# Kernel tuning notes

Measured on AMD Instinct MI355X. Metric: run time of the kernel, lower is better.

## Reference

```python
import jax, jax.numpy as jnp
import numpy as np

EPS = 1e-5
SCALE = 30.0

def _ln(x, g, b):
    m = jnp.mean(x, axis=-1, keepdims=True)
    v = jnp.mean((x - m) ** 2, axis=-1, keepdims=True)
    return (x - m) * jax.lax.rsqrt(v + EPS) * g + b

def setup_inputs() -> dict:
    key = jax.random.key(0)
    ks = jax.random.split(key, 12)
    B, L, K, H, NIN = 4, 2048, 48, 128, 512
    s = 0.02
    return {
        "h_V": jax.random.normal(ks[0], (B, L, H), jnp.float32),
        "h_E": jax.random.normal(ks[1], (B, L, K, NIN - H), jnp.float32),
        "mask_V": jnp.ones((B, L), jnp.float32),
        "mask_E": jnp.ones((B, L, K), jnp.float32),
        "w1": jax.random.normal(ks[2], (NIN, H), jnp.float32) * s,
        "b1": jnp.zeros((H,), jnp.float32),
        "w2": jax.random.normal(ks[3], (H, H), jnp.float32) * s,
        "b2": jnp.zeros((H,), jnp.float32),
        "w3": jax.random.normal(ks[4], (H, H), jnp.float32) * s,
        "b3": jnp.zeros((H,), jnp.float32),
        "g1": jnp.ones((H,), jnp.float32),
        "bn1": jnp.zeros((H,), jnp.float32),
        "g2": jnp.ones((H,), jnp.float32),
        "bn2": jnp.zeros((H,), jnp.float32),
        "wf1": jax.random.normal(ks[5], (H, 4 * H), jnp.float32) * s,
        "bf1": jnp.zeros((4 * H,), jnp.float32),
        "wf2": jax.random.normal(ks[6], (4 * H, H), jnp.float32) * s,
        "bf2": jnp.zeros((H,), jnp.float32),
    }

def reference(h_V, h_E, mask_V, mask_E, w1, b1, w2, b2, w3, b3, g1, bn1, g2, bn2, wf1, bf1, wf2, bf2):
    B, L, H = h_V.shape
    K = h_E.shape[-2]
    gelu = lambda x: jax.nn.gelu(x, approximate=False)  # torch nn.GELU default (erf)
    # expand source node over K neighbors and concat: (B,L,K,num_in)
    h_V_exp = jnp.broadcast_to(h_V[:, :, None, :], (B, L, K, H))
    h_EV = jnp.concatenate([h_V_exp, h_E], axis=-1)
    h_msg = gelu(jnp.einsum('blki,ih->blkh', h_EV, w1) + b1)
    h_msg = gelu(jnp.einsum('blkh,hj->blkj', h_msg, w2) + b2)
    h_msg = jnp.einsum('blkh,hj->blkj', h_msg, w3) + b3
    h_msg = mask_E[..., None] * h_msg
    dh = jnp.sum(h_msg, axis=-2) / SCALE  # masked sum-aggregate over K
    h = _ln(h_V + dh, g1, bn1)
    dff = jnp.einsum('blh,hf->blf', h, wf1) + bf1
    dff = jnp.einsum('blf,fh->blh', gelu(dff), wf2) + bf2
    h = _ln(h + dff, g2, bn2)
    return mask_V[..., None] * h
```

## Files before the change

kernel.cpp:

```cpp
#include <hip/hip_runtime.h>
#include <hip/hip_bf16.h>


typedef __bf16 bf16x8 __attribute__((ext_vector_type(8)));
typedef __bf16 bf16x4 __attribute__((ext_vector_type(4)));
typedef float f32x4 __attribute__((ext_vector_type(4)));

#define HH 128
#define EE 384
#define KK 48

__device__ __forceinline__ float gelu_f(float x) {
  float x2 = x * x;
  float u = x * (-1.5957691216f - 0.0713548163f * x2);
  float e = __expf(u);
  return __fdividef(x, 1.0f + e);
}

__device__ __forceinline__ bf16x8 cvt8v(f32x4 a, f32x4 b) {
  bf16x8 r;
  #pragma unroll
  for (int i = 0; i < 4; ++i) { r[i] = (__bf16)a[i]; r[i + 4] = (__bf16)b[i]; }
  return r;
}

__device__ __forceinline__ f32x4 mfma16(bf16x8 a, bf16x8 b, f32x4 c) {
  return __builtin_amdgcn_mfma_f32_16x16x32_bf16(a, b, c, 0, 0, 0);
}

__device__ __forceinline__ void gload16(const void* g, void* l) {
  __builtin_amdgcn_global_load_lds(
      (const __attribute__((address_space(1))) void*)g,
      (__attribute__((address_space(3))) void*)l, 16, 0, 0);
}

__global__ void prep_kernel(const float* __restrict__ w1, const float* __restrict__ w2,
                            const float* __restrict__ w3, const float* __restrict__ wf1,
                            const float* __restrict__ wf2, __bf16* __restrict__ out) {
  int idx = blockIdx.x * 256 + threadIdx.x;
  if (idx < 49152) {
    int t = idx & 7, lane = (idx >> 3) & 63, n = (idx >> 9) & 7, kc = idx >> 12;
    int e = kc * 32 + (lane >> 4) * 8 + t, h = n * 16 + (lane & 15);
    out[idx] = (__bf16)w1[(128 + e) * 128 + h];
  } else if (idx < 65536) {
    int u = idx - 49152;
    int t = u & 7, lane = (u >> 3) & 63, n = (u >> 9) & 7, kc = u >> 12;
    int e = kc * 32 + (lane >> 4) * 8 + t, h = n * 16 + (lane & 15);
    out[idx] = (__bf16)w2[e * 128 + h];
  } else if (idx < 81920) {
    int u = idx - 65536;
    int t = u & 7, lane = (u >> 3) & 63, n = (u >> 9) & 7, kc = u >> 12;
    int e = kc * 32 + (lane >> 4) * 8 + t, h = n * 16 + (lane & 15);
    out[idx] = (__bf16)w3[e * 128 + h];
  } else if (idx < 147456) {
    int u = idx - 81920;
    int t = u & 7, lane = (u >> 3) & 63, n = (u >> 9) & 7, kc = (u >> 12) & 3, w = u >> 14;
    int f = w * 128 + n * 16 + (lane & 15), h = kc * 32 + (lane >> 4) * 8 + t;
    out[idx] = (__bf16)wf1[h * 512 + f];
  } else if (idx < 212992) {
    int u = idx - 147456;
    int t = u & 7, lane = (u >> 3) & 63, n = (u >> 9) & 1, kc = (u >> 10) & 15, w = u >> 14;
    int j = w * 32 + n * 16 + (lane & 15), f = kc * 32 + (lane >> 4) * 8 + t;
    out[idx] = (__bf16)wf2[f * 128 + j];
  }
}

__global__ __launch_bounds__(128) void v1_kernel(const float* __restrict__ hV,
                                                 const float* __restrict__ w1,
                                                 const float* __restrict__ b1,
                                                 float* __restrict__ V1) {
  __shared__ __align__(16) float sV[16][128];
  const int tid = threadIdx.x;
  const long p0 = (long)blockIdx.x * 16;
  for (int i = 0; i < 16; ++i) sV[i][tid] = hV[(p0 + i) * HH + tid];
  __syncthreads();
  float acc[16];
  float bb = b1[tid];
  #pragma unroll
  for (int p = 0; p < 16; ++p) acc[p] = bb;
  for (int k = 0; k < 128; k += 4) {
    float wa = w1[(k + 0) * HH + tid];
    float wb = w1[(k + 1) * HH + tid];
    float wc = w1[(k + 2) * HH + tid];
    float wd = w1[(k + 3) * HH + tid];
    #pragma unroll
    for (int p = 0; p < 16; ++p) {
      float4 h4 = *(const float4*)&sV[p][k];
      acc[p] = fmaf(h4.x, wa, fmaf(h4.y, wb, fmaf(h4.z, wc, fmaf(h4.w, wd, acc[p]))));
    }
  }
  #pragma unroll
  for (int p = 0; p < 16; ++p) V1[(p0 + p) * HH + tid] = acc[p];
}

__global__ __launch_bounds__(256, 3) void msg_kernel(
    const float* __restrict__ hE, const float* __restrict__ hV,
    const float* __restrict__ maskE,
    const __bf16* __restrict__ w1f, const __bf16* __restrict__ w2f,
    const __bf16* __restrict__ w3f, const float* __restrict__ V1,
    const float* __restrict__ b2, const float* __restrict__ b3,
    const float* __restrict__ g1, const float* __restrict__ bn1,
    float* __restrict__ outH) {
  __shared__ __align__(16) char sBuf[3][12288];
  __shared__ __align__(16) float sBias[512];
  __shared__ __align__(16) float sPart[4][2];

  const int tid = threadIdx.x;
  const int lane = tid & 63;
  const int w = tid >> 6;
  const int fr = lane & 15;
  const int fg = lane >> 4;
  const long p = blockIdx.x;

  for (int j = tid; j < 512; j += 256) {
    float v;
    if (j < 128) v = b2[j];
    else if (j < 256) v = b3[j - 128];
    else if (j < 384) v = g1[j - 256];
    else v = bn1[j - 384];
    sBias[j] = v;
  }
  __syncthreads();

  const float mk0 = maskE[p * KK + fr];
  const float mk1 = maskE[p * KK + 16 + fr];
  const float mk2 = maskE[p * KK + 32 + fr];

  const char* hEp = (const char*)(hE + p * (long)(KK * EE));
  const int lrow = lane >> 4;
  const int lcb = (lane & 15) * 16;
  const int r0 = (w * 3 + 0) * 4 + lrow;
  const int r1 = (w * 3 + 1) * 4 + lrow;
  const int r2 = (w * 3 + 2) * 4 + lrow;
  const char* srcA0 = hEp + r0 * 1536 + (lcb ^ ((r0 & 7) << 5));
  const char* srcA1 = hEp + r1 * 1536 + (lcb ^ ((r1 & 7) << 5));
  const char* srcA2 = hEp + r2 * 1536 + (lcb ^ ((r2 & 7) << 5));
  const int dst0 = (w * 3 + 0) * 1024;
  const int dst1 = (w * 3 + 1) * 1024;
  const int dst2 = (w * 3 + 2) * 1024;

  const __bf16* b1base = w1f + (2 * w) * 512 + lane * 8;
  const __bf16* b2base = w2f + (2 * w) * 512 + lane * 8;
  const __bf16* b3base = w3f + (2 * w) * 512 + lane * 8;

  const int aswz = (fr & 7) << 5;
  const int hswz = (fr & 7) << 4;
  char* hB = &sBuf[0][0];

  f32x4 acc[3][2];
  #pragma unroll
  for (int m = 0; m < 3; ++m)
    #pragma unroll
    for (int n = 0; n < 2; ++n) acc[m][n] = (f32x4){0.f, 0.f, 0.f, 0.f};

  bf16x8 Bs0[2], Bs1[2], Bs2[2], Bs3[2];

#define STAGE(C, BUF) { \
    gload16(srcA0 + (C) * 256, &sBuf[BUF][0] + dst0); \
    gload16(srcA1 + (C) * 256, &sBuf[BUF][0] + dst1); \
    gload16(srcA2 + (C) * 256, &sBuf[BUF][0] + dst2); }
#define LOADB(SET, BASE, KC) { \
    SET[0] = *(const bf16x8*)((BASE) + (KC) * 4096); \
    SET[1] = *(const bf16x8*)((BASE) + (KC) * 4096 + 256); }
#define WAITV(N) asm volatile("s_waitcnt vmcnt(" #N ")" ::: "memory")
#define BAR      asm volatile("s_barrier" ::: "memory")
#define BARL     asm volatile("s_waitcnt lgkmcnt(0)\ns_barrier" ::: "memory")

#define KSTEP(BUF, KS, SET) { \
    const char* rb_ = &sBuf[BUF][0]; \
    const int cb_ = ((KS) * 128 + fg * 32) ^ aswz; \
    f32x4 x0_ = *(const f32x4*)(rb_ + fr * 256 + cb_); \
    f32x4 x1_ = *(const f32x4*)(rb_ + fr * 256 + cb_ + 16); \
    f32x4 x2_ = *(const f32x4*)(rb_ + (16 + fr) * 256 + cb_); \
    f32x4 x3_ = *(const f32x4*)(rb_ + (16 + fr) * 256 + cb_ + 16); \
    f32x4 x4_ = *(const f32x4*)(rb_ + (32 + fr) * 256 + cb_); \
    f32x4 x5_ = *(const f32x4*)(rb_ + (32 + fr) * 256 + cb_ + 16); \
    bf16x8 af0 = cvt8v(x0_, x1_); \
    bf16x8 af1 = cvt8v(x2_, x3_); \
    bf16x8 af2 = cvt8v(x4_, x5_); \
    acc[0][0] = mfma16(SET[0], af0, acc[0][0]); acc[0][1] = mfma16(SET[1], af0, acc[0][1]); \
    acc[1][0] = mfma16(SET[0], af1, acc[1][0]); acc[1][1] = mfma16(SET[1], af1, acc[1][1]); \
    acc[2][0] = mfma16(SET[0], af2, acc[2][0]); acc[2][1] = mfma16(SET[1], af2, acc[2][1]); }

#define KSTEPH(KS, SET) { \
    const int cb_ = ((KS) * 64 + fg * 16) ^ hswz; \
    bf16x8 af0 = *(const bf16x8*)(hB + fr * 256 + cb_); \
    bf16x8 af1 = *(const bf16x8*)(hB + (16 + fr) * 256 + cb_); \
    bf16x8 af2 = *(const bf16x8*)(hB + (32 + fr) * 256 + cb_); \
    acc[0][0] = mfma16(SET[0], af0, acc[0][0]); acc[0][1] = mfma16(SET[1], af0, acc[0][1]); \
    acc[1][0] = mfma16(SET[0], af1, acc[1][0]); acc[1][1] = mfma16(SET[1], af1, acc[1][1]); \
    acc[2][0] = mfma16(SET[0], af2, acc[2][0]); acc[2][1] = mfma16(SET[1], af2, acc[2][1]); }

#define EPI(BQ0, BQ1) { \
    _Pragma("unroll") for (int m_ = 0; m_ < 3; ++m_) { \
      const int rb_ = (m_ * 16 + fr) * 256; \
      { bf16x4 t_; \
        _Pragma("unroll") for (int j_ = 0; j_ < 4; ++j_) t_[j_] = (__bf16)gelu_f(acc[m_][0][j_] + BQ0[j_]); \
        *(bf16x4*)(hB + rb_ + (((2 * w) * 32 + fg * 8) ^ hswz)) = t_; \
        acc[m_][0] = (f32x4){0.f, 0.f, 0.f, 0.f}; } \
      { bf16x4 t_; \
        _Pragma("unroll") for (int j_ = 0; j_ < 4; ++j_) t_[j_] = (__bf16)gelu_f(acc[m_][1][j_] + BQ1[j_]); \
        *(bf16x4*)(hB + rb_ + (((2 * w + 1) * 32 + fg * 8) ^ hswz)) = t_; \
        acc[m_][1] = (f32x4){0.f, 0.f, 0.f, 0.f}; } } }

  STAGE(0, 0);
  LOADB(Bs0, b1base, 0);
  LOADB(Bs1, b1base, 1);
  STAGE(1, 1);
  LOADB(Bs2, b1base, 2);
  LOADB(Bs3, b1base, 3);

  f32x4 vq0, vq1, hq0, hq1;

  WAITV(7); BAR;
  KSTEP(0, 0, Bs0); LOADB(Bs0, b1base, 4);
  KSTEP(0, 1, Bs1); LOADB(Bs1, b1base, 5);
  STAGE(2, 2);

  WAITV(7); BAR;
  KSTEP(1, 0, Bs2); LOADB(Bs2, b1base, 6);
  KSTEP(1, 1, Bs3); LOADB(Bs3, b1base, 7);
  STAGE(3, 0);

  WAITV(7); BAR;
  KSTEP(2, 0, Bs0); LOADB(Bs0, b1base, 8);
  KSTEP(2, 1, Bs1); LOADB(Bs1, b1base, 9);
  STAGE(4, 1);

  WAITV(7); BAR;
  KSTEP(0, 0, Bs2); LOADB(Bs2, b1base, 10);
  KSTEP(0, 1, Bs3); LOADB(Bs3, b1base, 11);
  STAGE(5, 2);

  WAITV(7); BAR;
  KSTEP(1, 0, Bs0); LOADB(Bs0, b2base, 0);
  vq0 = *(const f32x4*)(V1 + p * HH + (2 * w) * 16 + fg * 4);
  vq1 = *(const f32x4*)(V1 + p * HH + (2 * w + 1) * 16 + fg * 4);
  KSTEP(1, 1, Bs1); LOADB(Bs1, b2base, 1);

  WAITV(6); BAR;
  KSTEP(2, 0, Bs2); LOADB(Bs2, b2base, 2);
  KSTEP(2, 1, Bs3); LOADB(Bs3, b2base, 3);

  WAITV(4);
  EPI(vq0, vq1);
  BARL;

  KSTEPH(0, Bs0); LOADB(Bs0, b3base, 0);
  KSTEPH(1, Bs1); LOADB(Bs1, b3base, 1);
  WAITV(4);
  KSTEPH(2, Bs2); LOADB(Bs2, b3base, 2);
  KSTEPH(3, Bs3); LOADB(Bs3, b3base, 3);
  BARL;
  {
    f32x4 bq0 = *(const f32x4*)(&sBias[(2 * w) * 16 + fg * 4]);
    f32x4 bq1 = *(const f32x4*)(&sBias[(2 * w + 1) * 16 + fg * 4]);
    EPI(bq0, bq1);
  }
  BARL;

  WAITV(6);
  KSTEPH(0, Bs0);
  hq0 = *(const f32x4*)(hV + p * HH + (2 * w) * 16 + fg * 4);
  hq1 = *(const f32x4*)(hV + p * HH + (2 * w + 1) * 16 + fg * 4);
  KSTEPH(1, Bs1);
  WAITV(4);
  KSTEPH(2, Bs2);
  KSTEPH(3, Bs3);

  f32x4 red[2];
  {
    #pragma unroll
    for (int n = 0; n < 2; ++n) {
      f32x4 bq = *(const f32x4*)(&sBias[128 + (2 * w + n) * 16 + fg * 4]);
      red[n] = mk0 * (acc[0][n] + bq) + mk1 * (acc[1][n] + bq) + mk2 * (acc[2][n] + bq);
    }
    #pragma unroll
    for (int off = 1; off <= 8; off <<= 1)
      #pragma unroll
      for (int n = 0; n < 2; ++n)
        #pragma unroll
        for (int j = 0; j < 4; ++j)
          red[n][j] += __shfl_xor(red[n][j], off);
  }

  WAITV(0);
  {
    f32x4 xq[2];
    xq[0] = hq0 + red[0] * (1.f / 30.f);
    xq[1] = hq1 + red[1] * (1.f / 30.f);
    float s = 0.f, t = 0.f;
    #pragma unroll
    for (int n = 0; n < 2; ++n)
      #pragma unroll
      for (int j = 0; j < 4; ++j) { float x = xq[n][j]; s += x; t += x * x; }
    s += __shfl_xor(s, 16); s += __shfl_xor(s, 32);
    t += __shfl_xor(t, 16); t += __shfl_xor(t, 32);
    if (lane == 0) { sPart[w][0] = s; sPart[w][1] = t; }
    BARL;
    float S = sPart[0][0] + sPart[1][0] + sPart[2][0] + sPart[3][0];
    float T = sPart[0][1] + sPart[1][1] + sPart[2][1] + sPart[3][1];
    float mean = S * (1.f / 128.f);
    float var = T * (1.f / 128.f) - mean * mean;
    float rs = rsqrtf(var + 1e-5f);
    if (fr == 0) {
      #pragma unroll
      for (int n = 0; n < 2; ++n) {
        f32x4 gq = *(const f32x4*)(&sBias[256 + (2 * w + n) * 16 + fg * 4]);
        f32x4 bq = *(const f32x4*)(&sBias[384 + (2 * w + n) * 16 + fg * 4]);
        f32x4 o;
        #pragma unroll
        for (int j = 0; j < 4; ++j) o[j] = (xq[n][j] - mean) * rs * gq[j] + bq[j];
        *(f32x4*)(outH + p * HH + (2 * w + n) * 16 + fg * 4) = o;
      }
    }
  }
#undef STAGE
#undef LOADB
#undef WAITV
#undef BAR
#undef BARL
#undef KSTEP
#undef KSTEPH
#undef EPI
}

__global__ __launch_bounds__(256, 2) void ffn_kernel(
    const float* __restrict__ xin, const __bf16* __restrict__ wf1g,
    const float* __restrict__ bf1, const __bf16* __restrict__ wf2g,
    const float* __restrict__ bf2, const float* __restrict__ g2,
    const float* __restrict__ bn2, const float* __restrict__ maskV,
    float* __restrict__ out) {
  __shared__ __align__(16) __bf16 sX[16][136];
  __shared__ __align__(16) __bf16 sH1[16][520];
  __shared__ __align__(16) float sOut[16][132];
  const int tid = threadIdx.x, lane = tid & 63, w = tid >> 6;
  const long row0 = (long)blockIdx.x * 16;
  const int fr = lane & 15, fg = lane >> 4;
  const __bf16* bw1 = wf1g + w * 16384 + lane * 8;
  const __bf16* bw2 = wf2g + w * 16384 + lane * 8;

  {
    int r = tid >> 4, c = (tid & 15) * 8;
    const float* src = xin + (row0 + r) * HH + c;
    f32x4 v0 = *(const f32x4*)src, v1 = *(const f32x4*)(src + 4);
    *(bf16x8*)&sX[r][c] = cvt8v(v0, v1);
  }
  __syncthreads();

  f32x4 a1[8];
  #pragma unroll
  for (int n = 0; n < 8; ++n) a1[n] = (f32x4){0.f, 0.f, 0.f, 0.f};
  #pragma unroll
  for (int kc = 0; kc < 4; ++kc) {
    int k0 = kc * 32;
    bf16x8 af0 = *(const bf16x8*)&sX[fr][k0 + fg * 8];
    #pragma unroll
    for (int n = 0; n < 8; ++n) {
      bf16x8 bfr = *(const bf16x8*)(bw1 + (kc * 8 + n) * 512);
      a1[n] = mfma16(af0, bfr, a1[n]);
    }
  }
  #pragma unroll
  for (int n = 0; n < 8; ++n) {
    float bv = bf1[w * 128 + n * 16 + fr];
    #pragma unroll
    for (int j = 0; j < 4; ++j)
      sH1[fg * 4 + j][w * 128 + n * 16 + fr] = (__bf16)gelu_f(a1[n][j] + bv);
  }
  __syncthreads();

  f32x4 a2[2];
  #pragma unroll
  for (int n = 0; n < 2; ++n) a2[n] = (f32x4){0.f, 0.f, 0.f, 0.f};
  #pragma unroll
  for (int kc = 0; kc < 16; ++kc) {
    int k0 = kc * 32;
    bf16x8 af0 = *(const bf16x8*)&sH1[fr][k0 + fg * 8];
    #pragma unroll
    for (int n = 0; n < 2; ++n) {
      bf16x8 bfr = *(const bf16x8*)(bw2 + (kc * 2 + n) * 512);
      a2[n] = mfma16(af0, bfr, a2[n]);
    }
  }
  #pragma unroll
  for (int n = 0; n < 2; ++n) {
    float bv = bf2[w * 32 + n * 16 + fr];
    #pragma unroll
    for (int j = 0; j < 4; ++j)
      sOut[fg * 4 + j][w * 32 + n * 16 + fr] = a2[n][j] + bv;
  }
  __syncthreads();

  {
    int r = tid >> 4, c0 = (tid & 15) * 8;
    long p = row0 + r;
    const float* xp = xin + p * HH + c0;
    float x[8];
    #pragma unroll
    for (int i = 0; i < 8; ++i) x[i] = xp[i] + sOut[r][c0 + i];
    float s = 0.f;
    #pragma unroll
    for (int i = 0; i < 8; ++i) s += x[i];
    s += __shfl_xor(s, 1); s += __shfl_xor(s, 2); s += __shfl_xor(s, 4); s += __shfl_xor(s, 8);
    float mean = s * (1.f / 128.f);
    float q = 0.f;
    #pragma unroll
    for (int i = 0; i < 8; ++i) { float e = x[i] - mean; q += e * e; }
    q += __shfl_xor(q, 1); q += __shfl_xor(q, 2); q += __shfl_xor(q, 4); q += __shfl_xor(q, 8);
    float rs = rsqrtf(q * (1.f / 128.f) + 1e-5f);
    float mv = maskV[p];
    float* op = out + p * HH + c0;
    #pragma unroll
    for (int i = 0; i < 8; ++i)
      op[i] = ((x[i] - mean) * rs * g2[c0 + i] + bn2[c0 + i]) * mv;
  }
}

extern "C" void kernel_launch(void* const* d_in, const int* in_sizes, int n_in,
                              void* d_out, int out_size, void* d_ws, size_t ws_size,
                              hipStream_t stream) {
  const float* hV    = (const float*)d_in[0];
  const float* hE    = (const float*)d_in[1];
  const float* maskV = (const float*)d_in[2];
  const float* maskE = (const float*)d_in[3];
  const float* w1    = (const float*)d_in[4];
  const float* b1    = (const float*)d_in[5];
  const float* w2    = (const float*)d_in[6];
  const float* b2    = (const float*)d_in[7];
  const float* w3    = (const float*)d_in[8];
  const float* b3    = (const float*)d_in[9];
  const float* g1    = (const float*)d_in[10];
  const float* bn1   = (const float*)d_in[11];
  const float* g2    = (const float*)d_in[12];
  const float* bn2   = (const float*)d_in[13];
  const float* wf1   = (const float*)d_in[14];
  const float* bf1   = (const float*)d_in[15];
  const float* wf2   = (const float*)d_in[16];
  const float* bf2   = (const float*)d_in[17];
  float* out = (float*)d_out;

  __bf16* wsb = (__bf16*)d_ws;
  float* V1   = (float*)((char*)d_ws + 425984);
  float* hbuf = (float*)((char*)d_ws + 4620288);

  prep_kernel<<<832, 256, 0, stream>>>(w1, w2, w3, wf1, wf2, wsb);
  v1_kernel<<<512, 128, 0, stream>>>(hV, w1, b1, V1);
  msg_kernel<<<8192, 256, 0, stream>>>(hE, hV, maskE,
                                       wsb, wsb + 49152, wsb + 65536, V1,
                                       b2, b3, g1, bn1, hbuf);
  ffn_kernel<<<512, 256, 0, stream>>>(hbuf, wsb + 81920, bf1, wsb + 147456, bf2,
                                      g2, bn2, maskV, out);
}
```

Before: 201.5 us.

## Process two nodes per msg block, prefetching second node's edges during first's tail

Each msg_kernel block now handles two consecutive nodes instead of one, halving the grid. The second node's h_E tiles are staged into the free LDS buffers while the first node's W2/W3 layers and LayerNorm run, so the global-load pipeline is not drained between nodes. LayerNorm switches from a one-pass E[x^2]-mean^2 variance to a two-pass centered variance, which adds an extra barrier. The hand-tuned vmcnt waits become more intricate, and the smaller grid means fewer blocks to spread across CUs.

```diff
diff --git a/kernel.cpp b/kernel.cpp
--- a/kernel.cpp
+++ b/kernel.cpp
@@ -110,7 +110,8 @@
   const int w = tid >> 6;
   const int fr = lane & 15;
   const int fg = lane >> 4;
-  const long p = blockIdx.x;
+  const long p0 = (long)blockIdx.x * 2;
+  const long p1 = p0 + 1;
 
   for (int j = tid; j < 512; j += 256) {
     float v;
@@ -122,11 +123,7 @@
   }
   __syncthreads();
 
-  const float mk0 = maskE[p * KK + fr];
-  const float mk1 = maskE[p * KK + 16 + fr];
-  const float mk2 = maskE[p * KK + 32 + fr];
-
-  const char* hEp = (const char*)(hE + p * (long)(KK * EE));
+  const char* hEp = (const char*)(hE + p0 * (long)(KK * EE));
   const int lrow = lane >> 4;
   const int lcb = (lane & 15) * 16;
   const int r0 = (w * 3 + 0) * 4 + lrow;
@@ -138,6 +135,7 @@
   const int dst0 = (w * 3 + 0) * 1024;
   const int dst1 = (w * 3 + 1) * 1024;
   const int dst2 = (w * 3 + 2) * 1024;
+  const int DP = KK * EE * 4;
 
   const __bf16* b1base = w1f + (2 * w) * 512 + lane * 8;
   const __bf16* b2base = w2f + (2 * w) * 512 + lane * 8;
@@ -145,7 +143,6 @@
 
   const int aswz = (fr & 7) << 5;
   const int hswz = (fr & 7) << 4;
-  char* hB = &sBuf[0][0];
 
   f32x4 acc[3][2];
   #pragma unroll
@@ -154,11 +151,12 @@
     for (int n = 0; n < 2; ++n) acc[m][n] = (f32x4){0.f, 0.f, 0.f, 0.f};
 
   bf16x8 Bs0[2], Bs1[2], Bs2[2], Bs3[2];
-
-#define STAGE(C, BUF) { \
-    gload16(srcA0 + (C) * 256, &sBuf[BUF][0] + dst0); \
-    gload16(srcA1 + (C) * 256, &sBuf[BUF][0] + dst1); \
-    gload16(srcA2 + (C) * 256, &sBuf[BUF][0] + dst2); }
+  float mk0, mk1, mk2;
+
+#define STAGE(POFF, C, BUF) { \
+    gload16(srcA0 + (POFF) + (C) * 256, &sBuf[BUF][0] + dst0); \
+    gload16(srcA1 + (POFF) + (C) * 256, &sBuf[BUF][0] + dst1); \
+    gload16(srcA2 + (POFF) + (C) * 256, &sBuf[BUF][0] + dst2); }
 #define LOADB(SET, BASE, KC) { \
     SET[0] = *(const bf16x8*)((BASE) + (KC) * 4096); \
     SET[1] = *(const bf16x8*)((BASE) + (KC) * 4096 + 256); }
@@ -182,139 +180,180 @@
     acc[1][0] = mfma16(SET[0], af1, acc[1][0]); acc[1][1] = mfma16(SET[1], af1, acc[1][1]); \
     acc[2][0] = mfma16(SET[0], af2, acc[2][0]); acc[2][1] = mfma16(SET[1], af2, acc[2][1]); }
 
-#define KSTEPH(KS, SET) { \
+#define KSTEPH(HB, KS, SET) { \
     const int cb_ = ((KS) * 64 + fg * 16) ^ hswz; \
-    bf16x8 af0 = *(const bf16x8*)(hB + fr * 256 + cb_); \
-    bf16x8 af1 = *(const bf16x8*)(hB + (16 + fr) * 256 + cb_); \
-    bf16x8 af2 = *(const bf16x8*)(hB + (32 + fr) * 256 + cb_); \
+    bf16x8 af0 = *(const bf16x8*)((HB) + fr * 256 + cb_); \
+    bf16x8 af1 = *(const bf16x8*)((HB) + (16 + fr) * 256 + cb_); \
+    bf16x8 af2 = *(const bf16x8*)((HB) + (32 + fr) * 256 + cb_); \
     acc[0][0] = mfma16(SET[0], af0, acc[0][0]); acc[0][1] = mfma16(SET[1], af0, acc[0][1]); \
     acc[1][0] = mfma16(SET[0], af1, acc[1][0]); acc[1][1] = mfma16(SET[1], af1, acc[1][1]); \
     acc[2][0] = mfma16(SET[0], af2, acc[2][0]); acc[2][1] = mfma16(SET[1], af2, acc[2][1]); }
 
-#define EPI(BQ0, BQ1) { \
+#define EPI(HB, BQ0, BQ1) { \
     _Pragma("unroll") for (int m_ = 0; m_ < 3; ++m_) { \
       const int rb_ = (m_ * 16 + fr) * 256; \
       { bf16x4 t_; \
         _Pragma("unroll") for (int j_ = 0; j_ < 4; ++j_) t_[j_] = (__bf16)gelu_f(acc[m_][0][j_] + BQ0[j_]); \
-        *(bf16x4*)(hB + rb_ + (((2 * w) * 32 + fg * 8) ^ hswz)) = t_; \
+        *(bf16x4*)((HB) + rb_ + (((2 * w) * 32 + fg * 8) ^ hswz)) = t_; \
         acc[m_][0] = (f32x4){0.f, 0.f, 0.f, 0.f}; } \
       { bf16x4 t_; \
         _Pragma("unroll") for (int j_ = 0; j_ < 4; ++j_) t_[j_] = (__bf16)gelu_f(acc[m_][1][j_] + BQ1[j_]); \
-        *(bf16x4*)(hB + rb_ + (((2 * w + 1) * 32 + fg * 8) ^ hswz)) = t_; \
+        *(bf16x4*)((HB) + rb_ + (((2 * w + 1) * 32 + fg * 8) ^ hswz)) = t_; \
         acc[m_][1] = (f32x4){0.f, 0.f, 0.f, 0.f}; } } }
 
-  STAGE(0, 0);
+#define REDLN(PP) { \
+    f32x4 red[2]; \
+    _Pragma("unroll") for (int n_ = 0; n_ < 2; ++n_) { \
+      f32x4 bq_ = *(const f32x4*)(&sBias[128 + (2 * w + n_) * 16 + fg * 4]); \
+      red[n_] = mk0 * (acc[0][n_] + bq_) + mk1 * (acc[1][n_] + bq_) + mk2 * (acc[2][n_] + bq_); \
+      acc[0][n_] = (f32x4){0.f, 0.f, 0.f, 0.f}; \
+      acc[1][n_] = (f32x4){0.f, 0.f, 0.f, 0.f}; \
+      acc[2][n_] = (f32x4){0.f, 0.f, 0.f, 0.f}; } \
+    _Pragma("unroll") for (int off_ = 1; off_ <= 8; off_ <<= 1) \
+      _Pragma("unroll") for (int n_ = 0; n_ < 2; ++n_) \
+        _Pragma("unroll") for (int j_ = 0; j_ < 4; ++j_) \
+          red[n_][j_] += __shfl_xor(red[n_][j_], off_); \
+    f32x4 xq[2]; \
+    xq[0] = hq0 + red[0] * (1.f / 30.f); \
+    xq[1] = hq1 + red[1] * (1.f / 30.f); \
+    float s_ = 0.f; \
+    _Pragma("unroll") for (int n_ = 0; n_ < 2; ++n_) \
+      _Pragma("unroll") for (int j_ = 0; j_ < 4; ++j_) s_ += xq[n_][j_]; \
+    s_ += __shfl_xor(s_, 16); s_ += __shfl_xor(s_, 32); \
+    if (lane == 0) sPart[w][0] = s_; \
+    BARL; \
+    float mean_ = (sPart[0][0] + sPart[1][0] + sPart[2][0] + sPart[3][0]) * (1.f / 128.f); \
+    float q_ = 0.f; \
+    _Pragma("unroll") for (int n_ = 0; n_ < 2; ++n_) \
+      _Pragma("unroll") for (int j_ = 0; j_ < 4; ++j_) { float e_ = xq[n_][j_] - mean_; q_ += e_ * e_; } \
+    q_ += __shfl_xor(q_, 16); q_ += __shfl_xor(q_, 32); \
+    if (lane == 0) sPart[w][1] = q_; \
+    BARL; \
+    float var_ = (sPart[0][1] + sPart[1][1] + sPart[2][1] + sPart[3][1]) * (1.f / 128.f); \
+    float rs_ = rsqrtf(var_ + 1e-5f); \
+    if (fr == 0) { \
+      _Pragma("unroll") for (int n_ = 0; n_ < 2; ++n_) { \
+        f32x4 gq_ = *(const f32x4*)(&sBias[256 + (2 * w + n_) * 16 + fg * 4]); \
+        f32x4 bq_ = *(const f32x4*)(&sBias[384 + (2 * w + n_) * 16 + fg * 4]); \
+        f32x4 o_; \
+        _Pragma("unroll") for (int j_ = 0; j_ < 4; ++j_) \
+          o_[j_] = (xq[n_][j_] - mean_) * rs_ * gq_[j_] + bq_[j_]; \
+        *(f32x4*)(outH + (PP) * HH + (2 * w + n_) * 16 + fg * 4) = o_; } } }
+
+  f32x4 vq0, vq1, hq0, hq1;
+
+  mk0 = maskE[p0 * KK + fr]; mk1 = maskE[p0 * KK + 16 + fr]; mk2 = maskE[p0 * KK + 32 + fr];
+  STAGE(0, 0, 0);
   LOADB(Bs0, b1base, 0);
   LOADB(Bs1, b1base, 1);
-  STAGE(1, 1);
+  STAGE(0, 1, 1);
   LOADB(Bs2, b1base, 2);
   LOADB(Bs3, b1base, 3);
 
-  f32x4 vq0, vq1, hq0, hq1;
-
   WAITV(7); BAR;
   KSTEP(0, 0, Bs0); LOADB(Bs0, b1base, 4);
   KSTEP(0, 1, Bs1); LOADB(Bs1, b1base, 5);
-  STAGE(2, 2);
-
+  STAGE(0, 2, 2);
   WAITV(7); BAR;
   KSTEP(1, 0, Bs2); LOADB(Bs2, b1base, 6);
   KSTEP(1, 1, Bs3); LOADB(Bs3, b1base, 7);
-  STAGE(3, 0);
-
+  STAGE(0, 3, 0);
   WAITV(7); BAR;
   KSTEP(2, 0, Bs0); LOADB(Bs0, b1base, 8);
   KSTEP(2, 1, Bs1); LOADB(Bs1, b1base, 9);
-  STAGE(4, 1);
-
+  STAGE(0, 4, 1);
   WAITV(7); BAR;
   KSTEP(0, 0, Bs2); LOADB(Bs2, b1base, 10);
   KSTEP(0, 1, Bs3); LOADB(Bs3, b1base, 11);
-  STAGE(5, 2);
-
+  STAGE(0, 5, 2);
   WAITV(7); BAR;
   KSTEP(1, 0, Bs0); LOADB(Bs0, b2base, 0);
-  vq0 = *(const f32x4*)(V1 + p * HH + (2 * w) * 16 + fg * 4);
-  vq1 = *(const f32x4*)(V1 + p * HH + (2 * w + 1) * 16 + fg * 4);
+  vq0 = *(const f32x4*)(V1 + p0 * HH + (2 * w) * 16 + fg * 4);
+  vq1 = *(const f32x4*)(V1 + p0 * HH + (2 * w + 1) * 16 + fg * 4);
   KSTEP(1, 1, Bs1); LOADB(Bs1, b2base, 1);
-
   WAITV(6); BAR;
   KSTEP(2, 0, Bs2); LOADB(Bs2, b2base, 2);
   KSTEP(2, 1, Bs3); LOADB(Bs3, b2base, 3);
 
-  WAITV(4);
-  EPI(vq0, vq1);
-  BARL;
-
-  KSTEPH(0, Bs0); LOADB(Bs0, b3base, 0);
-  KSTEPH(1, Bs1); LOADB(Bs1, b3base, 1);
-  WAITV(4);
-  KSTEPH(2, Bs2); LOADB(Bs2, b3base, 2);
-  KSTEPH(3, Bs3); LOADB(Bs3, b3base, 3);
+  WAITV(6);
+  EPI(&sBuf[0][0], vq0, vq1);
+  BARL;
+  STAGE(DP, 0, 1);
+
+  KSTEPH(&sBuf[0][0], 0, Bs0); LOADB(Bs0, b3base, 0);
+  hq0 = *(const f32x4*)(hV + p0 * HH + (2 * w) * 16 + fg * 4);
+  hq1 = *(const f32x4*)(hV + p0 * HH + (2 * w + 1) * 16 + fg * 4);
+  WAITV(11); KSTEPH(&sBuf[0][0], 1, Bs1); LOADB(Bs1, b3base, 1);
+  WAITV(11); KSTEPH(&sBuf[0][0], 2, Bs2); LOADB(Bs2, b3base, 2);
+  WAITV(11); KSTEPH(&sBuf[0][0], 3, Bs3); LOADB(Bs3, b3base, 3);
   BARL;
   {
     f32x4 bq0 = *(const f32x4*)(&sBias[(2 * w) * 16 + fg * 4]);
     f32x4 bq1 = *(const f32x4*)(&sBias[(2 * w + 1) * 16 + fg * 4]);
-    EPI(bq0, bq1);
-  }
-  BARL;
+    EPI(&sBuf[0][0], bq0, bq1);
+  }
+  BARL;
+  STAGE(DP, 1, 2);
+
+  WAITV(11); KSTEPH(&sBuf[0][0], 0, Bs0); LOADB(Bs0, b1base, 0);
+  WAITV(9);  KSTEPH(&sBuf[0][0], 1, Bs1); LOADB(Bs1, b1base, 1);
+  WAITV(9);  KSTEPH(&sBuf[0][0], 2, Bs2); LOADB(Bs2, b1base, 2);
+  WAITV(9);  KSTEPH(&sBuf[0][0], 3, Bs3); LOADB(Bs3, b1base, 3);
+
+  REDLN(p0);
+
+  mk0 = maskE[p1 * KK + fr]; mk1 = maskE[p1 * KK + 16 + fr]; mk2 = maskE[p1 * KK + 32 + fr];
+  STAGE(DP, 2, 0);
+
+  WAITV(10); BAR;
+  KSTEP(1, 0, Bs0); LOADB(Bs0, b1base, 4);
+  KSTEP(1, 1, Bs1); LOADB(Bs1, b1base, 5);
+  WAITV(10); BAR;
+  KSTEP(2, 0, Bs2); LOADB(Bs2, b1base, 6);
+  KSTEP(2, 1, Bs3); LOADB(Bs3, b1base, 7);
+  STAGE(DP, 3, 1);
+  WAITV(7); BAR;
+  KSTEP(0, 0, Bs0); LOADB(Bs0, b1base, 8);
+  KSTEP(0, 1, Bs1); LOADB(Bs1, b1base, 9);
+  STAGE(DP, 4, 2);
+  WAITV(7); BAR;
+  KSTEP(1, 0, Bs2); LOADB(Bs2, b1base, 10);
+  KSTEP(1, 1, Bs3); LOADB(Bs3, b1base, 11);
+  STAGE(DP, 5, 0);
+  WAITV(7); BAR;
+  KSTEP(2, 0, Bs0); LOADB(Bs0, b2base, 0);
+  vq0 = *(const f32x4*)(V1 + p1 * HH + (2 * w) * 16 + fg * 4);
+  vq1 = *(const f32x4*)(V1 + p1 * HH + (2 * w + 1) * 16 + fg * 4);
+  KSTEP(2, 1, Bs1); LOADB(Bs1, b2base, 1);
+  WAITV(6); BAR;
+  KSTEP(0, 0, Bs2); LOADB(Bs2, b2base, 2);
+  KSTEP(0, 1, Bs3); LOADB(Bs3, b2base, 3);
 
   WAITV(6);
-  KSTEPH(0, Bs0);
-  hq0 = *(const f32x4*)(hV + p * HH + (2 * w) * 16 + fg * 4);
-  hq1 = *(const f32x4*)(hV + p * HH + (2 * w + 1) * 16 + fg * 4);
-  KSTEPH(1, Bs1);
-  WAITV(4);
-  KSTEPH(2, Bs2);
-  KSTEPH(3, Bs3);
-
-  f32x4 red[2];
+  EPI(&sBuf[1][0], vq0, vq1);
+  BARL;
+
+  KSTEPH(&sBuf[1][0], 0, Bs0); LOADB(Bs0, b3base, 0);
+  hq0 = *(const f32x4*)(hV + p1 * HH + (2 * w) * 16 + fg * 4);
+  hq1 = *(const f32x4*)(hV + p1 * HH + (2 * w + 1) * 16 + fg * 4);
+  WAITV(8); KSTEPH(&sBuf[1][0], 1, Bs1); LOADB(Bs1, b3base, 1);
+  WAITV(8); KSTEPH(&sBuf[1][0], 2, Bs2); LOADB(Bs2, b3base, 2);
+  WAITV(8); KSTEPH(&sBuf[1][0], 3, Bs3); LOADB(Bs3, b3base, 3);
+  BARL;
   {
-    #pragma unroll
-    for (int n = 0; n < 2; ++n) {
-      f32x4 bq = *(const f32x4*)(&sBias[128 + (2 * w + n) * 16 + fg * 4]);
-      red[n] = mk0 * (acc[0][n] + bq) + mk1 * (acc[1][n] + bq) + mk2 * (acc[2][n] + bq);
-    }
-    #pragma unroll
-    for (int off = 1; off <= 8; off <<= 1)
-      #pragma unroll
-      for (int n = 0; n < 2; ++n)
-        #pragma unroll
-        for (int j = 0; j < 4; ++j)
-          red[n][j] += __shfl_xor(red[n][j], off);
-  }
-
-  WAITV(0);
-  {
-    f32x4 xq[2];
-    xq[0] = hq0 + red[0] * (1.f / 30.f);
-    xq[1] = hq1 + red[1] * (1.f / 30.f);
-    float s = 0.f, t = 0.f;
-    #pragma unroll
-    for (int n = 0; n < 2; ++n)
-      #pragma unroll
-      for (int j = 0; j < 4; ++j) { float x = xq[n][j]; s += x; t += x * x; }
-    s += __shfl_xor(s, 16); s += __shfl_xor(s, 32);
-    t += __shfl_xor(t, 16); t += __shfl_xor(t, 32);
-    if (lane == 0) { sPart[w][0] = s; sPart[w][1] = t; }
-    BARL;
-    float S = sPart[0][0] + sPart[1][0] + sPart[2][0] + sPart[3][0];
-    float T = sPart[0][1] + sPart[1][1] + sPart[2][1] + sPart[3][1];
-    float mean = S * (1.f / 128.f);
-    float var = T * (1.f / 128.f) - mean * mean;
-    float rs = rsqrtf(var + 1e-5f);
-    if (fr == 0) {
-      #pragma unroll
-      for (int n = 0; n < 2; ++n) {
-        f32x4 gq = *(const f32x4*)(&sBias[256 + (2 * w + n) * 16 + fg * 4]);
-        f32x4 bq = *(const f32x4*)(&sBias[384 + (2 * w + n) * 16 + fg * 4]);
-        f32x4 o;
-        #pragma unroll
-        for (int j = 0; j < 4; ++j) o[j] = (xq[n][j] - mean) * rs * gq[j] + bq[j];
-        *(f32x4*)(outH + p * HH + (2 * w + n) * 16 + fg * 4) = o;
-      }
-    }
-  }
+    f32x4 bq0 = *(const f32x4*)(&sBias[(2 * w) * 16 + fg * 4]);
+    f32x4 bq1 = *(const f32x4*)(&sBias[(2 * w + 1) * 16 + fg * 4]);
+    EPI(&sBuf[1][0], bq0, bq1);
+  }
+  BARL;
+
+  WAITV(8); KSTEPH(&sBuf[1][0], 0, Bs0);
+  WAITV(4); KSTEPH(&sBuf[1][0], 1, Bs1);
+  WAITV(2); KSTEPH(&sBuf[1][0], 2, Bs2);
+  WAITV(0); KSTEPH(&sBuf[1][0], 3, Bs3);
+
+  REDLN(p1);
+
 #undef STAGE
 #undef LOADB
 #undef WAITV
@@ -323,6 +362,7 @@
 #undef KSTEP
 #undef KSTEPH
 #undef EPI
+#undef REDLN
 }
 
 __global__ __launch_bounds__(256, 2) void ffn_kernel(
@@ -446,7 +486,7 @@
 
   prep_kernel<<<832, 256, 0, stream>>>(w1, w2, w3, wf1, wf2, wsb);
   v1_kernel<<<512, 128, 0, stream>>>(hV, w1, b1, V1);
-  msg_kernel<<<8192, 256, 0, stream>>>(hE, hV, maskE,
+  msg_kernel<<<4096, 256, 0, stream>>>(hE, hV, maskE,
                                        wsb, wsb + 49152, wsb + 65536, V1,
                                        b2, b3, g1, bn1, hbuf);
   ffn_kernel<<<512, 256, 0, stream>>>(hbuf, wsb + 81920, bf1, wsb + 147456, bf2,
```

After: 216.2 us. 7.3% more time.
